# Performance work log

Hardware: AMD Instinct MI355X
Metric: run time of the kernel (lower is better)

Reference implementation:

```python
import jax, jax.numpy as jnp
import numpy as np
import itertools

N_LEVELS = 16
F = 2
OFFSETS = [0, 4096, 12096, 27721, 60489, 124489, 249489, 511633, 1023633,
           1547921, 2072209, 2596497, 3120785, 3645073, 4169361, 4693649, 5217937]
RESOLUTIONS = [16, 20, 25, 32, 40, 50, 64, 80, 101, 128, 161, 203, 256, 322, 406, 512]
# Instant-NGP spatial hash primes (first prime = 1)
PRIMES = np.array([1, 2654435761, 805459861], dtype=np.uint32)
CORNERS = np.array(list(itertools.product([0, 1], repeat=3)), dtype=np.int32)  # (8,3)
B = 1 << 20


def setup_inputs() -> dict:
    key = jax.random.key(0)
    k1, k2 = jax.random.split(key)
    xyz = jax.random.uniform(k1, (B, 3), dtype=jnp.float32)  # points in [0,1)
    embeddings = jax.random.normal(k2, (OFFSETS[-1], F), dtype=jnp.float32) * 0.01
    return {
        'xyz': xyz,
        'embeddings': embeddings,
        'min_xyz': jnp.zeros((3,), jnp.float32),
        'max_xyz': jnp.ones((3,), jnp.float32),
    }


def _hashgrid_encode(xyz, embeddings, min_xyz, max_xyz):
    # normalize to [0,1] inside the grid bbox
    xyz_n = (xyz - min_xyz) / (max_xyz - min_xyz)  # (B,3)
    corners_u = jnp.asarray(CORNERS).astype(jnp.uint32)          # (8,3)
    corners_f = jnp.asarray(CORNERS).astype(jnp.float32)         # (8,3)
    primes = jnp.asarray(PRIMES)                                  # (3,) uint32
    outs = []
    for l in range(N_LEVELS):
        res = RESOLUTIONS[l]
        size = OFFSETS[l + 1] - OFFSETS[l]
        pos = xyz_n * (res - 1)                                   # (B,3) in [0,res-1]
        pos0 = jnp.clip(jnp.floor(pos), 0.0, res - 2)             # lower corner
        w = pos - pos0                                            # (B,3) trilinear frac
        p0 = pos0.astype(jnp.uint32)
        idx3 = p0[:, None, :] + corners_u[None]                   # (B,8,3)
        if res ** 3 <= size:
            # dense level: linear index
            idx = idx3[..., 0] * jnp.uint32(res * res) + idx3[..., 1] * jnp.uint32(res) + idx3[..., 2]
        else:
            # hashed level: xor of prime-multiplied coords (uint32 wraparound)
            idx = (idx3[..., 0] * primes[0]) ^ (idx3[..., 1] * primes[1]) ^ (idx3[..., 2] * primes[2])
            idx = idx % jnp.uint32(size)
        idx = idx.astype(jnp.int32) + OFFSETS[l]                  # (B,8) global entry id
        # trilinear weights: prod_d [ c_d ? w_d : 1-w_d ]
        wc = jnp.prod(corners_f[None] * w[:, None, :] + (1.0 - corners_f[None]) * (1.0 - w[:, None, :]), axis=-1)  # (B,8)
        feats = embeddings[idx]                                   # (B,8,F) gather
        outs.append(jnp.einsum('bc,bcf->bf', wc, feats))          # (B,F)
    return jnp.concatenate(outs, axis=-1)                         # (B, L*F)


def reference(xyz, embeddings, min_xyz, max_xyz):
    return _hashgrid_encode(xyz, embeddings, min_xyz, max_xyz)
```

## Files before the change

### kernel.cpp

```cpp
#include <hip/hip_runtime.h>
#include <stdint.h>


typedef float vf4 __attribute__((ext_vector_type(4)));
typedef float vf2 __attribute__((ext_vector_type(2)));

__device__ __constant__ int kRES[16] = {16,20,25,32,40,50,64,80,101,128,161,203,256,322,406,512};

#define D_RES   {16,20,25,32,40,50,64,80}
#define D_OFF   {0u,4096u,12096u,27721u,60489u,124489u,249489u,511633u}
#define D_CBASE {0u,3375u,10234u,24058u,53849u,113168u,230817u,480864u}
#define D_CTOT  973903u
#define PREP_MAXTASK 1972156u

template<int RES, uint32_t OFF, uint32_t CBASE>
__device__ __forceinline__ void prep_level(const float2* __restrict__ emb,
                                           float2* __restrict__ ws,
                                           uint32_t tid)
{
    constexpr uint32_t r1 = (uint32_t)(RES - 1);
    constexpr uint32_t ntask = r1 * r1 * r1 * 4u;
    if (tid >= ntask) return;

    const uint32_t cell = tid >> 2;
    const uint32_t part = tid & 3u;

    const uint32_t cz = cell % r1;
    const uint32_t t  = cell / r1;
    const uint32_t cy = t % r1;
    const uint32_t cx = t / r1;

    const uint32_t bx = part >> 1, by = part & 1u;
    const uint32_t src = OFF + (cx + bx) * (uint32_t)(RES * RES)
                             + (cy + by) * (uint32_t)RES + cz;

    const float2 e0 = emb[src];
    const float2 e1 = emb[src + 1];

    vf4 v = {e0.x, e0.y, e1.x, e1.y};
    __builtin_nontemporal_store(v, (vf4*)(ws + ((size_t)(CBASE + cell) * 8u + part * 2u)));
}

__global__ __launch_bounds__(256) void prep_cells(
    const float2* __restrict__ emb, float2* __restrict__ ws)
{
    const uint32_t tid = blockIdx.x * 256u + threadIdx.x;
    switch (blockIdx.y) {
        case 0: prep_level<16,      0u,      0u>(emb, ws, tid); break;
        case 1: prep_level<20,   4096u,   3375u>(emb, ws, tid); break;
        case 2: prep_level<25,  12096u,  10234u>(emb, ws, tid); break;
        case 3: prep_level<32,  27721u,  24058u>(emb, ws, tid); break;
        case 4: prep_level<40,  60489u,  53849u>(emb, ws, tid); break;
        case 5: prep_level<50, 124489u, 113168u>(emb, ws, tid); break;
        case 6: prep_level<64, 249489u, 230817u>(emb, ws, tid); break;
        case 7: prep_level<80, 511633u, 480864u>(emb, ws, tid); break;
    }
}

__device__ __forceinline__ float2 hash_level(const float2* __restrict__ emb,
                                             int l, float xn, float yn, float zn)
{
    constexpr uint32_t P1 = 2654435761u, P2 = 805459861u;
    constexpr uint32_t HASH_MASK = 0x7FFFFu;
    constexpr uint32_t HASH_BASE = 1023633u;

    const int res = kRES[l];
    const uint32_t off = HASH_BASE + (uint32_t)(l - 8) * 524288u;

    const float scale = (float)(res - 1);
    const float hi    = (float)(res - 2);

    const float px = xn * scale, py = yn * scale, pz = zn * scale;
    const float fx = fminf(fmaxf(floorf(px), 0.0f), hi);
    const float fy = fminf(fmaxf(floorf(py), 0.0f), hi);
    const float fz = fminf(fmaxf(floorf(pz), 0.0f), hi);
    const float wx1 = px - fx, wy1 = py - fy, wz1 = pz - fz;
    const float wx0 = 1.0f - wx1, wy0 = 1.0f - wy1, wz0 = 1.0f - wz1;
    const uint32_t ix = (uint32_t)fx, iy = (uint32_t)fy, iz = (uint32_t)fz;

    const uint32_t hx0 = ix,      hx1 = ix + 1u;
    const uint32_t hy0 = iy * P1, hy1 = hy0 + P1;
    const uint32_t hz0 = iz * P2, hz1 = hz0 + P2;

    const uint32_t i000 = ((hx0 ^ hy0 ^ hz0) & HASH_MASK) + off;
    const uint32_t i001 = ((hx0 ^ hy0 ^ hz1) & HASH_MASK) + off;
    const uint32_t i010 = ((hx0 ^ hy1 ^ hz0) & HASH_MASK) + off;
    const uint32_t i011 = ((hx0 ^ hy1 ^ hz1) & HASH_MASK) + off;
    const uint32_t i100 = ((hx1 ^ hy0 ^ hz0) & HASH_MASK) + off;
    const uint32_t i101 = ((hx1 ^ hy0 ^ hz1) & HASH_MASK) + off;
    const uint32_t i110 = ((hx1 ^ hy1 ^ hz0) & HASH_MASK) + off;
    const uint32_t i111 = ((hx1 ^ hy1 ^ hz1) & HASH_MASK) + off;

    const float2 e000 = emb[i000], e001 = emb[i001], e010 = emb[i010], e011 = emb[i011];
    const float2 e100 = emb[i100], e101 = emb[i101], e110 = emb[i110], e111 = emb[i111];

    float ax, ay, w;
    w = wx0 * wy0 * wz0; ax  = w * e000.x; ay  = w * e000.y;
    w = wx0 * wy0 * wz1; ax += w * e001.x; ay += w * e001.y;
    w = wx0 * wy1 * wz0; ax += w * e010.x; ay += w * e010.y;
    w = wx0 * wy1 * wz1; ax += w * e011.x; ay += w * e011.y;
    w = wx1 * wy0 * wz0; ax += w * e100.x; ay += w * e100.y;
    w = wx1 * wy0 * wz1; ax += w * e101.x; ay += w * e101.y;
    w = wx1 * wy1 * wz0; ax += w * e110.x; ay += w * e110.y;
    w = wx1 * wy1 * wz1; ax += w * e111.x; ay += w * e111.y;
    return make_float2(ax, ay);
}

__global__ __launch_bounds__(256, 8) void hashgrid_cell(
    const float* __restrict__ xyz,
    const float2* __restrict__ emb,
    const float2* __restrict__ ws,
    const float* __restrict__ mn,
    const float* __restrict__ mx,
    float* __restrict__ out,
    int npts)
{
    const int b = blockIdx.x * blockDim.x + threadIdx.x;
    if (b >= npts) return;

    const float mn0 = mn[0], mn1 = mn[1], mn2 = mn[2];
    const float inv0 = 1.0f / (mx[0] - mn0);
    const float inv1 = 1.0f / (mx[1] - mn1);
    const float inv2 = 1.0f / (mx[2] - mn2);

    const float xn = (__builtin_nontemporal_load(&xyz[3 * b + 0]) - mn0) * inv0;
    const float yn = (__builtin_nontemporal_load(&xyz[3 * b + 1]) - mn1) * inv1;
    const float zn = (__builtin_nontemporal_load(&xyz[3 * b + 2]) - mn2) * inv2;

    const int y = blockIdx.y;

    if (y == 0) {
        constexpr int RES[8] = D_RES;
        constexpr uint32_t CB[8] = D_CBASE;
        float o[16];
#pragma unroll
        for (int l = 0; l < 8; ++l) {
            const int res = RES[l];
            const uint32_t r1 = (uint32_t)(res - 1);
            const float scale = (float)(res - 1);
            const float hi    = (float)(res - 2);

            const float px = xn * scale, py = yn * scale, pz = zn * scale;
            const float fx = fminf(fmaxf(floorf(px), 0.0f), hi);
            const float fy = fminf(fmaxf(floorf(py), 0.0f), hi);
            const float fz = fminf(fmaxf(floorf(pz), 0.0f), hi);
            const float wx1 = px - fx, wy1 = py - fy, wz1 = pz - fz;
            const float wx0 = 1.0f - wx1, wy0 = 1.0f - wy1, wz0 = 1.0f - wz1;
            const uint32_t ix = (uint32_t)fx, iy = (uint32_t)fy, iz = (uint32_t)fz;

            const uint32_t cell = CB[l] + (ix * r1 + iy) * r1 + iz;
            const vf4* blk = (const vf4*)(ws + (size_t)cell * 8u);
            const vf4 q0 = blk[0], q1 = blk[1], q2 = blk[2], q3 = blk[3];

            float ax, ay, w;
            w = wx0 * wy0; ax  = w * (wz0 * q0.x + wz1 * q0.z); ay  = w * (wz0 * q0.y + wz1 * q0.w);
            w = wx0 * wy1; ax += w * (wz0 * q1.x + wz1 * q1.z); ay += w * (wz0 * q1.y + wz1 * q1.w);
            w = wx1 * wy0; ax += w * (wz0 * q2.x + wz1 * q2.z); ay += w * (wz0 * q2.y + wz1 * q2.w);
            w = wx1 * wy1; ax += w * (wz0 * q3.x + wz1 * q3.z); ay += w * (wz0 * q3.y + wz1 * q3.w);
            o[2 * l]     = ax;
            o[2 * l + 1] = ay;
        }
        float* op = out + (size_t)b * 32;
#pragma unroll
        for (int i = 0; i < 4; ++i) {
            vf4 v = {o[4 * i + 0], o[4 * i + 1], o[4 * i + 2], o[4 * i + 3]};
            __builtin_nontemporal_store(v, (vf4*)(op + 4 * i));
        }
    } else {
        const int l0 = 6 + 2 * y;
        const float2 ra = hash_level(emb, l0,     xn, yn, zn);
        const float2 rb = hash_level(emb, l0 + 1, xn, yn, zn);
        vf4 v = {ra.x, ra.y, rb.x, rb.y};
        __builtin_nontemporal_store(v, (vf4*)(out + (size_t)b * 32 + 2 * l0));
    }
}

__global__ __launch_bounds__(256, 8) void hashgrid_direct(
    const float* __restrict__ xyz,
    const float2* __restrict__ emb,
    const float* __restrict__ mn,
    const float* __restrict__ mx,
    float* __restrict__ out,
    int npts)
{
    const int b = blockIdx.x * blockDim.x + threadIdx.x;
    if (b >= npts) return;

    const float mn0 = mn[0], mn1 = mn[1], mn2 = mn[2];
    const float inv0 = 1.0f / (mx[0] - mn0);
    const float inv1 = 1.0f / (mx[1] - mn1);
    const float inv2 = 1.0f / (mx[2] - mn2);

    const float xn = (xyz[3 * b + 0] - mn0) * inv0;
    const float yn = (xyz[3 * b + 1] - mn1) * inv1;
    const float zn = (xyz[3 * b + 2] - mn2) * inv2;

    const int y = blockIdx.y;

    if (y == 0) {
        constexpr int RES[8] = D_RES;
        constexpr uint32_t OFFS[8] = D_OFF;
        float o[16];
#pragma unroll
        for (int l = 0; l < 8; ++l) {
            const int res = RES[l];
            const uint32_t off = OFFS[l];
            const float scale = (float)(res - 1);
            const float hi = (float)(res - 2);

            const float px = xn * scale, py = yn * scale, pz = zn * scale;
            const float fx = fminf(fmaxf(floorf(px), 0.0f), hi);
            const float fy = fminf(fmaxf(floorf(py), 0.0f), hi);
            const float fz = fminf(fmaxf(floorf(pz), 0.0f), hi);
            const float wx1 = px - fx, wy1 = py - fy, wz1 = pz - fz;
            const float wx0 = 1.0f - wx1, wy0 = 1.0f - wy1, wz0 = 1.0f - wz1;
            const uint32_t ix = (uint32_t)fx, iy = (uint32_t)fy, iz = (uint32_t)fz;

            const uint32_t dx = (uint32_t)(res * res);
            const uint32_t dy = (uint32_t)res;
            const uint32_t base = off + ix * dx + iy * dy + iz;

            float ax = 0.0f, ay = 0.0f;
            {
                float2 e0 = emb[base];           float2 e1 = emb[base + 1];
                float wxy = wx0 * wy0;
                ax += wxy * (wz0 * e0.x + wz1 * e1.x); ay += wxy * (wz0 * e0.y + wz1 * e1.y);
            }
            {
                float2 e0 = emb[base + dy];      float2 e1 = emb[base + dy + 1];
                float wxy = wx0 * wy1;
                ax += wxy * (wz0 * e0.x + wz1 * e1.x); ay += wxy * (wz0 * e0.y + wz1 * e1.y);
            }
            {
                float2 e0 = emb[base + dx];      float2 e1 = emb[base + dx + 1];
                float wxy = wx1 * wy0;
                ax += wxy * (wz0 * e0.x + wz1 * e1.x); ay += wxy * (wz0 * e0.y + wz1 * e1.y);
            }
            {
                float2 e0 = emb[base + dx + dy]; float2 e1 = emb[base + dx + dy + 1];
                float wxy = wx1 * wy1;
                ax += wxy * (wz0 * e0.x + wz1 * e1.x); ay += wxy * (wz0 * e0.y + wz1 * e1.y);
            }
            o[2 * l]     = ax;
            o[2 * l + 1] = ay;
        }
        float4* ov = (float4*)(out + (size_t)b * 32);
#pragma unroll
        for (int i = 0; i < 4; ++i)
            ov[i] = make_float4(o[4 * i + 0], o[4 * i + 1], o[4 * i + 2], o[4 * i + 3]);
    } else {
        const int l0 = 6 + 2 * y;
        const float2 ra = hash_level(emb, l0,     xn, yn, zn);
        const float2 rb = hash_level(emb, l0 + 1, xn, yn, zn);
        float4* op = (float4*)(out + (size_t)b * 32 + 2 * l0);
        *op = make_float4(ra.x, ra.y, rb.x, rb.y);
    }
}

extern "C" void kernel_launch(void* const* d_in, const int* in_sizes, int n_in,
                              void* d_out, int out_size, void* d_ws, size_t ws_size,
                              hipStream_t stream) {
    const float*  xyz = (const float*)d_in[0];
    const float2* emb = (const float2*)d_in[1];
    const float*  mn  = (const float*)d_in[2];
    const float*  mx  = (const float*)d_in[3];
    float* out = (float*)d_out;

    const int npts = in_sizes[0] / 3;
    const int block = 256;
    const int grid_x = (npts + block - 1) / block;

    const size_t ws_needed = (size_t)D_CTOT * 64u;

    if (ws_size >= ws_needed && d_ws != nullptr) {
        float2* ws = (float2*)d_ws;
        const int prep_gx = (int)((PREP_MAXTASK + 255u) / 256u);
        hipLaunchKernelGGL(prep_cells, dim3(prep_gx, 8), dim3(256), 0, stream, emb, ws);
        hipLaunchKernelGGL(hashgrid_cell, dim3(grid_x, 5), dim3(block), 0, stream,
                           xyz, emb, ws, mn, mx, out, npts);
    } else {
        hipLaunchKernelGGL(hashgrid_direct, dim3(grid_x, 5), dim3(block), 0, stream,
                           xyz, emb, mn, mx, out, npts);
    }
}
```

Measured before the change: 738.5 us.

## Merge level-group grid slices into one thread per point handling all levels

Removes the 5-way blockIdx.y split so that each thread computes all 16 levels for its point: the 8 dense levels from the precomputed cell table, then the 8 hashed levels in an unrolled loop. This loads and normalises xyz once instead of five times and writes each output row from a single thread, trading away the parallelism across levels. Launch bounds drop to 6 waves per SIMD to leave room for the larger register footprint, which lowers occupancy for a gather-heavy, latency-bound kernel.

```diff
diff --git a/kernel.cpp b/kernel.cpp
--- a/kernel.cpp
+++ b/kernel.cpp
@@ -106,7 +106,7 @@
     return make_float2(ax, ay);
 }
 
-__global__ __launch_bounds__(256, 8) void hashgrid_cell(
+__global__ __launch_bounds__(256, 6) void hashgrid_mono(
     const float* __restrict__ xyz,
     const float2* __restrict__ emb,
     const float2* __restrict__ ws,
@@ -127,9 +127,9 @@
     const float yn = (__builtin_nontemporal_load(&xyz[3 * b + 1]) - mn1) * inv1;
     const float zn = (__builtin_nontemporal_load(&xyz[3 * b + 2]) - mn2) * inv2;
 
-    const int y = blockIdx.y;
-
-    if (y == 0) {
+    float* op = out + (size_t)b * 32;
+
+    {
         constexpr int RES[8] = D_RES;
         constexpr uint32_t CB[8] = D_CBASE;
         float o[16];
@@ -160,22 +160,24 @@
             o[2 * l]     = ax;
             o[2 * l + 1] = ay;
         }
-        float* op = out + (size_t)b * 32;
 #pragma unroll
         for (int i = 0; i < 4; ++i) {
             vf4 v = {o[4 * i + 0], o[4 * i + 1], o[4 * i + 2], o[4 * i + 3]};
             __builtin_nontemporal_store(v, (vf4*)(op + 4 * i));
         }
-    } else {
-        const int l0 = 6 + 2 * y;
+    }
+
+#pragma unroll
+    for (int p = 0; p < 4; ++p) {
+        const int l0 = 8 + 2 * p;
         const float2 ra = hash_level(emb, l0,     xn, yn, zn);
         const float2 rb = hash_level(emb, l0 + 1, xn, yn, zn);
         vf4 v = {ra.x, ra.y, rb.x, rb.y};
-        __builtin_nontemporal_store(v, (vf4*)(out + (size_t)b * 32 + 2 * l0));
-    }
-}
-
-__global__ __launch_bounds__(256, 8) void hashgrid_direct(
+        __builtin_nontemporal_store(v, (vf4*)(op + 16 + 4 * p));
+    }
+}
+
+__global__ __launch_bounds__(256, 6) void hashgrid_mono_direct(
     const float* __restrict__ xyz,
     const float2* __restrict__ emb,
     const float* __restrict__ mn,
@@ -195,9 +197,9 @@
     const float yn = (xyz[3 * b + 1] - mn1) * inv1;
     const float zn = (xyz[3 * b + 2] - mn2) * inv2;
 
-    const int y = blockIdx.y;
-
-    if (y == 0) {
+    float* op = out + (size_t)b * 32;
+
+    {
         constexpr int RES[8] = D_RES;
         constexpr uint32_t OFFS[8] = D_OFF;
         float o[16];
@@ -244,16 +246,19 @@
             o[2 * l]     = ax;
             o[2 * l + 1] = ay;
         }
-        float4* ov = (float4*)(out + (size_t)b * 32);
+        float4* ov = (float4*)op;
 #pragma unroll
         for (int i = 0; i < 4; ++i)
             ov[i] = make_float4(o[4 * i + 0], o[4 * i + 1], o[4 * i + 2], o[4 * i + 3]);
-    } else {
-        const int l0 = 6 + 2 * y;
+    }
+
+#pragma unroll
+    for (int p = 0; p < 4; ++p) {
+        const int l0 = 8 + 2 * p;
         const float2 ra = hash_level(emb, l0,     xn, yn, zn);
         const float2 rb = hash_level(emb, l0 + 1, xn, yn, zn);
-        float4* op = (float4*)(out + (size_t)b * 32 + 2 * l0);
-        *op = make_float4(ra.x, ra.y, rb.x, rb.y);
+        float4* ov = (float4*)(op + 16 + 4 * p);
+        *ov = make_float4(ra.x, ra.y, rb.x, rb.y);
     }
 }
 
@@ -276,10 +281,10 @@
         float2* ws = (float2*)d_ws;
         const int prep_gx = (int)((PREP_MAXTASK + 255u) / 256u);
         hipLaunchKernelGGL(prep_cells, dim3(prep_gx, 8), dim3(256), 0, stream, emb, ws);
-        hipLaunchKernelGGL(hashgrid_cell, dim3(grid_x, 5), dim3(block), 0, stream,
+        hipLaunchKernelGGL(hashgrid_mono, dim3(grid_x), dim3(block), 0, stream,
                            xyz, emb, ws, mn, mx, out, npts);
     } else {
-        hipLaunchKernelGGL(hashgrid_direct, dim3(grid_x, 5), dim3(block), 0, stream,
+        hipLaunchKernelGGL(hashgrid_mono_direct, dim3(grid_x), dim3(block), 0, stream,
                            xyz, emb, mn, mx, out, npts);
     }
 }
```

After: 864.8 us. +17.1%, slower.
